# Kernel tuning notes

Hardware: AMD Instinct MI355X
Metric: run time of the kernel (lower is better)

## Reference

```python
import jax, jax.numpy as jnp
import numpy as np

A, V, T = 32, 32, 128          # per-modality hidden dims
PF = 128                       # post_fusion_dim
FUSED = (A + 1) * (V + 1) * (T + 1)  # 140481
B = 256


def setup_inputs() -> dict:
    key = jax.random.key(0)
    ks = jax.random.split(key, 9)
    s1 = 1.0 / np.sqrt(FUSED)
    s2 = 1.0 / np.sqrt(PF)
    return {
        "audio_x": jax.random.normal(ks[0], (B, A), dtype=jnp.float32),
        "video_x": jax.random.normal(ks[1], (B, V), dtype=jnp.float32),
        "text_x": jax.random.normal(ks[2], (B, T), dtype=jnp.float32),
        "W1": jax.random.uniform(ks[3], (FUSED, PF), jnp.float32, -s1, s1),
        "b1": jax.random.uniform(ks[4], (PF,), jnp.float32, -s1, s1),
        "W2": jax.random.uniform(ks[5], (PF, PF), jnp.float32, -s2, s2),
        "b2": jax.random.uniform(ks[6], (PF,), jnp.float32, -s2, s2),
        "W3": jax.random.uniform(ks[7], (PF, 1), jnp.float32, -s2, s2),
        "b3": jax.random.uniform(ks[8], (1,), jnp.float32, -s2, s2),
    }


def reference(audio_x, video_x, text_x, W1, b1, W2, b2, W3, b3):
    b = audio_x.shape[0]
    ones = jnp.ones((b, 1), dtype=audio_x.dtype)
    a = jnp.concatenate([ones, audio_x], axis=1)  # (B, A+1)
    v = jnp.concatenate([ones, video_x], axis=1)  # (B, V+1)
    t = jnp.concatenate([ones, text_x], axis=1)   # (B, T+1)
    # trilinear outer product, flattened: (B, (A+1)*(V+1)*(T+1))
    fusion = jnp.einsum("ba,bv,bt->bavt", a, v, t).reshape(b, -1)
    h1 = jax.nn.relu(fusion @ W1 + b1)
    h2 = jax.nn.relu(h1 @ W2 + b2)
    return h2 @ W3 + b3
```

## Files before the change

### kernel.cpp

```cpp
#include <hip/hip_runtime.h>
#include <hip/hip_bf16.h>
#include <stdint.h>

#define BATCH 256
#define PFD 128
#define T1 129
#define NPAIRS 1089
#define BK2 136
#define CHUNK 8

typedef short bf16x8 __attribute__((ext_vector_type(8)));
typedef float f32x4 __attribute__((ext_vector_type(4)));

static __device__ __forceinline__ float float_of(unsigned u){ union{float f;unsigned u;}x;x.u=u;return x.f; }
static __device__ __forceinline__ unsigned pk_bf16(float a, float b){
  union { __hip_bfloat162 h; unsigned u; } c;
  c.h = __float22bfloat162_rn(make_float2(a, b));
  return c.u;
}

static __device__ __forceinline__ void gl_lds16(const float* g, float* l) {
  __builtin_amdgcn_global_load_lds(
      (const __attribute__((address_space(1))) unsigned int*)g,
      (__attribute__((address_space(3))) unsigned int*)l,
      16, 0, 0);
}

__global__ __launch_bounds__(512, 2) void tfn_k1(
    const float* __restrict__ audio, const float* __restrict__ video,
    const float* __restrict__ text, const float* __restrict__ W1,
    unsigned short* __restrict__ part, int S) {
  __shared__ __align__(16) float w_lds[128 * 128];
  __shared__ __align__(16) short b_lds[PFD * BK2];
  __shared__ __align__(16) float av_lds[BATCH * CHUNK];

  const int tid = threadIdx.x;
  const int bk = blockIdx.x;
  const int npb = NPAIRS / S, rem0 = NPAIRS % S;
  const int p0 = bk * npb + (bk < rem0 ? bk : rem0);
  const int np = npb + (bk < rem0 ? 1 : 0);

  const int wave = tid >> 6, lane = tid & 63;
  const int l15 = lane & 15, quad = lane >> 4;
  const int sn = tid & 127, skg = tid >> 7;

  float treg[2][32];
  float t128r[2];
  #pragma unroll
  for (int mt = 0; mt < 2; ++mt) {
    const int m = wave * 32 + mt * 16 + l15;
    t128r[mt] = text[m * 128 + 127];
    #pragma unroll
    for (int ks = 0; ks < 4; ++ks)
      #pragma unroll
      for (int j = 0; j < 8; ++j) {
        const int it = ks * 32 + quad * 8 + j;
        treg[mt][ks * 8 + j] = (it == 0) ? 1.0f : text[m * 128 + it - 1];
      }
  }

  f32x4 acc[2][8];
  #pragma unroll
  for (int a = 0; a < 2; ++a)
    #pragma unroll
    for (int b = 0; b < 8; ++b) acc[a][b] = f32x4{0.f, 0.f, 0.f, 0.f};

  float rv[8];

  for (int c0 = 0; c0 < np; c0 += CHUNK) {
    const int nc = (np - c0) < CHUNK ? (np - c0) : CHUNK;
    const int pbase = p0 + c0;
    __syncthreads();
    if (tid < BATCH) {
      const int m = tid;
      for (int j = 0; j < nc; ++j) {
        int p = pbase + j;
        int ia = p / 33, iv = p - ia * 33;
        float a = (ia == 0) ? 1.0f : audio[m * 32 + ia - 1];
        float v = (iv == 0) ? 1.0f : video[m * 32 + iv - 1];
        av_lds[m * CHUNK + j] = a * v;
      }
    }
    #pragma unroll
    for (int j = 0; j < 8; ++j) {
      int kk = skg * 8 + j;
      rv[j] = (kk < nc) ? W1[((long)(pbase + kk) * T1 + 128) * PFD + sn] : 0.0f;
    }
    {
      const float* gsrc = W1 + (long)pbase * (T1 * PFD);
      #pragma unroll
      for (int g = 0; g < 8; ++g)
        gl_lds16(gsrc + g * 2048 + wave * 256 + lane * 4,
                 &w_lds[g * 2048 + wave * 256]);
    }
    for (int sp = 0; sp < nc; ++sp) {
      __syncthreads();
      {
        union { bf16x8 v; unsigned u[4]; } w;
        #pragma unroll
        for (int g = 0; g < 4; ++g) {
          float f[8];
          #pragma unroll
          for (int j = 0; j < 8; ++j)
            f[j] = w_lds[(g * 32 + skg * 8 + j) * 128 + sn];
          #pragma unroll
          for (int d = 0; d < 4; ++d) w.u[d] = pk_bf16(f[2 * d], f[2 * d + 1]);
          *(bf16x8*)&b_lds[sn * BK2 + g * 32 + skg * 8] = w.v;
        }
      }
      __syncthreads();
      if (sp + 1 < nc) {
        const float* gsrc = W1 + (long)(pbase + sp + 1) * (T1 * PFD);
        #pragma unroll
        for (int g = 0; g < 8; ++g)
          gl_lds16(gsrc + g * 2048 + wave * 256 + lane * 4,
                   &w_lds[g * 2048 + wave * 256]);
      }
      const float avm0 = av_lds[(wave * 32 + l15) * CHUNK + sp];
      const float avm1 = av_lds[(wave * 32 + 16 + l15) * CHUNK + sp];
      #pragma unroll
      for (int ks = 0; ks < 4; ++ks) {
        bf16x8 A0, A1;
        {
          union { bf16x8 v; unsigned u[4]; } c0u, c1u;
          #pragma unroll
          for (int d = 0; d < 4; ++d) {
            c0u.u[d] = pk_bf16(avm0 * treg[0][ks * 8 + 2 * d], avm0 * treg[0][ks * 8 + 2 * d + 1]);
            c1u.u[d] = pk_bf16(avm1 * treg[1][ks * 8 + 2 * d], avm1 * treg[1][ks * 8 + 2 * d + 1]);
          }
          A0 = c0u.v; A1 = c1u.v;
        }
        #pragma unroll
        for (int nt = 0; nt < 8; ++nt) {
          bf16x8 bf = *(const bf16x8*)&b_lds[(nt * 16 + l15) * BK2 + ks * 32 + quad * 8];
          acc[0][nt] = __builtin_amdgcn_mfma_f32_16x16x32_bf16(A0, bf, acc[0][nt], 0, 0, 0);
          acc[1][nt] = __builtin_amdgcn_mfma_f32_16x16x32_bf16(A1, bf, acc[1][nt], 0, 0, 0);
        }
      }
    }
    __syncthreads();
    {
      union { bf16x8 v; unsigned u[4]; } w;
      #pragma unroll
      for (int d = 0; d < 4; ++d) w.u[d] = pk_bf16(rv[2 * d], rv[2 * d + 1]);
      *(bf16x8*)&b_lds[sn * BK2 + skg * 8] = w.v;
    }
    __syncthreads();
    {
      bf16x8 A[2];
      #pragma unroll
      for (int mt = 0; mt < 2; ++mt) {
        const int m = wave * 32 + mt * 16 + l15;
        union { bf16x8 v; unsigned u[4]; } c;
        #pragma unroll
        for (int d = 0; d < 4; ++d) {
          int k0 = quad * 8 + 2 * d, k1 = k0 + 1;
          float f0 = (k0 < nc) ? av_lds[m * CHUNK + k0] * t128r[mt] : 0.0f;
          float f1 = (k1 < nc) ? av_lds[m * CHUNK + k1] * t128r[mt] : 0.0f;
          c.u[d] = pk_bf16(f0, f1);
        }
        A[mt] = c.v;
      }
      #pragma unroll
      for (int nt = 0; nt < 8; ++nt) {
        bf16x8 bf = *(const bf16x8*)&b_lds[(nt * 16 + l15) * BK2 + quad * 8];
        acc[0][nt] = __builtin_amdgcn_mfma_f32_16x16x32_bf16(A[0], bf, acc[0][nt], 0, 0, 0);
        acc[1][nt] = __builtin_amdgcn_mfma_f32_16x16x32_bf16(A[1], bf, acc[1][nt], 0, 0, 0);
      }
    }
  }

  #pragma unroll
  for (int mt = 0; mt < 2; ++mt)
    #pragma unroll
    for (int r = 0; r < 4; ++r) {
      const int m = wave * 32 + mt * 16 + quad * 4 + r;
      union { bf16x8 v; unsigned u[4]; } w;
      #pragma unroll
      for (int d = 0; d < 4; ++d) w.u[d] = pk_bf16(acc[mt][2 * d][r], acc[mt][2 * d + 1][r]);
      *(bf16x8*)&part[((size_t)m * S + bk) * PFD + l15 * 8] = w.v;
    }
}

__global__ __launch_bounds__(1024) void tfn_k2(
    const unsigned short* __restrict__ part, const float* __restrict__ b1,
    const float* __restrict__ W2, const float* __restrict__ b2,
    const float* __restrict__ W3, const float* __restrict__ b3,
    float* __restrict__ out, int S) {
  __shared__ float sred[1024 * 4];
  __shared__ float h1s[PFD];
  __shared__ float a2s[1024];
  __shared__ float red[2];
  const int m = blockIdx.x, tid = threadIdx.x;
  const int g = tid & 31, q = tid >> 5;
  const unsigned short* base = part + (size_t)m * S * PFD;
  float s0 = 0, s1 = 0, s2 = 0, s3 = 0;
  for (int bkk = q; bkk < S; bkk += 32) {
    uint2 v = *(const uint2*)&base[(size_t)bkk * PFD + g * 4];
    s0 += float_of(v.x << 16);
    s1 += float_of(v.x & 0xFFFF0000u);
    s2 += float_of(v.y << 16);
    s3 += float_of(v.y & 0xFFFF0000u);
  }
  sred[tid * 4 + 0] = s0; sred[tid * 4 + 1] = s1;
  sred[tid * 4 + 2] = s2; sred[tid * 4 + 3] = s3;
  __syncthreads();
  if (tid < PFD) {
    const int p = tid;
    float h = 0;
    #pragma unroll
    for (int bl = 0; bl < 32; ++bl) h += sred[(bl * 32 + (p >> 2)) * 4 + (p & 3)];
    const int n = (p & 7) * 16 + (p >> 3);
    h1s[n] = fmaxf(h + b1[n], 0.0f);
  }
  __syncthreads();
  const int n = tid & 127, kq = tid >> 7;
  float a2 = 0.0f;
  const int k0 = kq * 16;
  #pragma unroll
  for (int k = 0; k < 16; ++k) a2 += h1s[k0 + k] * W2[(k0 + k) * PFD + n];
  a2s[tid] = a2;
  __syncthreads();
  if (tid < 128) {
    float h2 = 0.0f;
    #pragma unroll
    for (int j = 0; j < 8; ++j) h2 += a2s[n + 128 * j];
    h2 = fmaxf(h2 + b2[n], 0.0f);
    float pr = h2 * W3[n];
    #pragma unroll
    for (int off = 32; off > 0; off >>= 1) pr += __shfl_down(pr, off);
    if ((tid & 63) == 0) red[tid >> 6] = pr;
  }
  __syncthreads();
  if (tid == 0) out[m] = red[0] + red[1] + b3[0];
}

extern "C" void kernel_launch(void* const* d_in, const int* in_sizes, int n_in,
                              void* d_out, int out_size, void* d_ws, size_t ws_size,
                              hipStream_t stream) {
  const float* audio = (const float*)d_in[0];
  const float* video = (const float*)d_in[1];
  const float* text  = (const float*)d_in[2];
  const float* W1 = (const float*)d_in[3];
  const float* b1 = (const float*)d_in[4];
  const float* W2 = (const float*)d_in[5];
  const float* b2 = (const float*)d_in[6];
  const float* W3 = (const float*)d_in[7];
  const float* b3 = (const float*)d_in[8];
  unsigned short* part = (unsigned short*)d_ws;

  const size_t slab = (size_t)BATCH * PFD * sizeof(unsigned short);
  int S = (int)(ws_size / slab);
  if (S > 256) S = 256;
  if (S < 1) S = 1;

  tfn_k1<<<S, 512, 0, stream>>>(audio, video, text, W1, part, S);
  tfn_k2<<<BATCH, 1024, 0, stream>>>(part, b1, W2, b2, W3, b3, (float*)d_out, S);
}
```

Measured before the change: 137.2 us.

## Double-buffer W1 half-slices in LDS with explicit waitcnt-based pipelining

Splits each 128-row W1 slice into two 64-row halves and keeps two LDS buffers for both the fp32 staging data and the bf16 B tile. The async global-to-LDS load for step s+2 is issued while step s is converted and multiplied. Explicit vmcnt waits and raw s_barrier replace __syncthreads, so the DMA can overlap with MFMA work instead of being exposed. This adds more barriers per pair, and the hand-written waitcnt counts must match the number of outstanding loads to stay correct.

```diff
diff --git a/kernel.cpp b/kernel.cpp
--- a/kernel.cpp
+++ b/kernel.cpp
@@ -6,7 +6,7 @@
 #define PFD 128
 #define T1 129
 #define NPAIRS 1089
-#define BK2 136
+#define BH 72
 #define CHUNK 8
 
 typedef short bf16x8 __attribute__((ext_vector_type(8)));
@@ -30,8 +30,8 @@
     const float* __restrict__ audio, const float* __restrict__ video,
     const float* __restrict__ text, const float* __restrict__ W1,
     unsigned short* __restrict__ part, int S) {
-  __shared__ __align__(16) float w_lds[128 * 128];
-  __shared__ __align__(16) short b_lds[PFD * BK2];
+  __shared__ __align__(16) float w_lds[2][64 * 128];
+  __shared__ __align__(16) short b_lds[2][PFD * BH];
   __shared__ __align__(16) float av_lds[BATCH * CHUNK];
 
   const int tid = threadIdx.x;
@@ -86,64 +86,77 @@
       int kk = skg * 8 + j;
       rv[j] = (kk < nc) ? W1[((long)(pbase + kk) * T1 + 128) * PFD + sn] : 0.0f;
     }
-    {
-      const float* gsrc = W1 + (long)pbase * (T1 * PFD);
-      #pragma unroll
-      for (int g = 0; g < 8; ++g)
+
+    auto dma_half = [&](int s, int hb) {
+      const float* gsrc = W1 + (long)(pbase + (s >> 1)) * (T1 * PFD) + (s & 1) * (64 * PFD);
+      #pragma unroll
+      for (int g = 0; g < 4; ++g)
         gl_lds16(gsrc + g * 2048 + wave * 256 + lane * 4,
-                 &w_lds[g * 2048 + wave * 256]);
-    }
-    for (int sp = 0; sp < nc; ++sp) {
-      __syncthreads();
+                 &w_lds[hb][g * 2048 + wave * 256]);
+    };
+
+    dma_half(0, 0);
+    dma_half(1, 1);
+
+    const int NS = 2 * nc;
+    for (int s = 0; s < NS; ++s) {
+      const int hb = s & 1;
+      if (s == NS - 1) { asm volatile("s_waitcnt vmcnt(0) lgkmcnt(0)"); }
+      else             { asm volatile("s_waitcnt vmcnt(4) lgkmcnt(0)"); }
+      __builtin_amdgcn_sched_barrier(0);
+      __builtin_amdgcn_s_barrier();
+      __builtin_amdgcn_sched_barrier(0);
       {
         union { bf16x8 v; unsigned u[4]; } w;
         #pragma unroll
-        for (int g = 0; g < 4; ++g) {
+        for (int g = 0; g < 2; ++g) {
           float f[8];
           #pragma unroll
           for (int j = 0; j < 8; ++j)
-            f[j] = w_lds[(g * 32 + skg * 8 + j) * 128 + sn];
+            f[j] = w_lds[hb][(g * 32 + skg * 8 + j) * 128 + sn];
           #pragma unroll
           for (int d = 0; d < 4; ++d) w.u[d] = pk_bf16(f[2 * d], f[2 * d + 1]);
-          *(bf16x8*)&b_lds[sn * BK2 + g * 32 + skg * 8] = w.v;
+          *(bf16x8*)&b_lds[hb][sn * BH + g * 32 + skg * 8] = w.v;
         }
       }
-      __syncthreads();
-      if (sp + 1 < nc) {
-        const float* gsrc = W1 + (long)(pbase + sp + 1) * (T1 * PFD);
+      asm volatile("s_waitcnt lgkmcnt(0)");
+      __builtin_amdgcn_sched_barrier(0);
+      __builtin_amdgcn_s_barrier();
+      __builtin_amdgcn_sched_barrier(0);
+      if (s + 2 < NS) dma_half(s + 2, hb);
+      {
+        const int sp = s >> 1, h = s & 1;
+        const float avm0 = av_lds[(wave * 32 + l15) * CHUNK + sp];
+        const float avm1 = av_lds[(wave * 32 + 16 + l15) * CHUNK + sp];
         #pragma unroll
-        for (int g = 0; g < 8; ++g)
-          gl_lds16(gsrc + g * 2048 + wave * 256 + lane * 4,
-                   &w_lds[g * 2048 + wave * 256]);
-      }
-      const float avm0 = av_lds[(wave * 32 + l15) * CHUNK + sp];
-      const float avm1 = av_lds[(wave * 32 + 16 + l15) * CHUNK + sp];
-      #pragma unroll
-      for (int ks = 0; ks < 4; ++ks) {
-        bf16x8 A0, A1;
-        {
-          union { bf16x8 v; unsigned u[4]; } c0u, c1u;
+        for (int ksl = 0; ksl < 2; ++ksl) {
+          const int ks = h * 2 + ksl;
+          bf16x8 A0, A1;
+          {
+            union { bf16x8 v; unsigned u[4]; } c0u, c1u;
+            #pragma unroll
+            for (int d = 0; d < 4; ++d) {
+              c0u.u[d] = pk_bf16(avm0 * treg[0][ks * 8 + 2 * d], avm0 * treg[0][ks * 8 + 2 * d + 1]);
+              c1u.u[d] = pk_bf16(avm1 * treg[1][ks * 8 + 2 * d], avm1 * treg[1][ks * 8 + 2 * d + 1]);
+            }
+            A0 = c0u.v; A1 = c1u.v;
+          }
           #pragma unroll
-          for (int d = 0; d < 4; ++d) {
-            c0u.u[d] = pk_bf16(avm0 * treg[0][ks * 8 + 2 * d], avm0 * treg[0][ks * 8 + 2 * d + 1]);
-            c1u.u[d] = pk_bf16(avm1 * treg[1][ks * 8 + 2 * d], avm1 * treg[1][ks * 8 + 2 * d + 1]);
+          for (int nt = 0; nt < 8; ++nt) {
+            bf16x8 bf = *(const bf16x8*)&b_lds[hb][(nt * 16 + l15) * BH + ksl * 32 + quad * 8];
+            acc[0][nt] = __builtin_amdgcn_mfma_f32_16x16x32_bf16(A0, bf, acc[0][nt], 0, 0, 0);
+            acc[1][nt] = __builtin_amdgcn_mfma_f32_16x16x32_bf16(A1, bf, acc[1][nt], 0, 0, 0);
           }
-          A0 = c0u.v; A1 = c1u.v;
         }
-        #pragma unroll
-        for (int nt = 0; nt < 8; ++nt) {
-          bf16x8 bf = *(const bf16x8*)&b_lds[(nt * 16 + l15) * BK2 + ks * 32 + quad * 8];
-          acc[0][nt] = __builtin_amdgcn_mfma_f32_16x16x32_bf16(A0, bf, acc[0][nt], 0, 0, 0);
-          acc[1][nt] = __builtin_amdgcn_mfma_f32_16x16x32_bf16(A1, bf, acc[1][nt], 0, 0, 0);
-        }
-      }
-    }
+      }
+    }
+
     __syncthreads();
     {
       union { bf16x8 v; unsigned u[4]; } w;
       #pragma unroll
       for (int d = 0; d < 4; ++d) w.u[d] = pk_bf16(rv[2 * d], rv[2 * d + 1]);
-      *(bf16x8*)&b_lds[sn * BK2 + skg * 8] = w.v;
+      *(bf16x8*)&b_lds[0][sn * BH + skg * 8] = w.v;
     }
     __syncthreads();
     {
@@ -163,7 +176,7 @@
       }
       #pragma unroll
       for (int nt = 0; nt < 8; ++nt) {
-        bf16x8 bf = *(const bf16x8*)&b_lds[(nt * 16 + l15) * BK2 + quad * 8];
+        bf16x8 bf = *(const bf16x8*)&b_lds[0][(nt * 16 + l15) * BH + quad * 8];
         acc[0][nt] = __builtin_amdgcn_mfma_f32_16x16x32_bf16(A[0], bf, acc[0][nt], 0, 0, 0);
         acc[1][nt] = __builtin_amdgcn_mfma_f32_16x16x32_bf16(A[1], bf, acc[1][nt], 0, 0, 0);
       }
```

Measured after the change: 167.9 us. +22.4%, slower.
